# Kernel tuning notes

Measured on AMD Instinct MI355X. Metric: run time of the kernel, lower is better.

The kernel has to match this reference:

```python
import jax, jax.numpy as jnp
import numpy as np

N = 50000
E = 1600000
IN_C = 128
HID_C = 128
OUT_C = 64
NUM_REL = 8
NUM_BASES = 4


def rgcn_conv(x, edge_index, edge_type, basis, comp, root, bias):
    """Faithful PyG RGCNConv with basis decomposition and mean aggregation.

    basis: (num_bases, in, out); comp: (num_rel, num_bases);
    root: (in, out); bias: (out,).
    """
    # Compose per-relation weights from bases: W_r = sum_b comp[r,b] * basis[b]
    W = jnp.einsum('rb,bio->rio', comp, basis)  # (R, in, out)
    src, dst = edge_index[0], edge_index[1]
    # Segment id encodes (relation, dst node) so one segment_sum handles all relations
    seg = edge_type * N + dst  # (E,)
    msgs = x[src]  # (E, in) gather
    sums = jax.ops.segment_sum(msgs, seg, num_segments=NUM_REL * N)
    cnt = jax.ops.segment_sum(jnp.ones((seg.shape[0],), dtype=x.dtype), seg,
                              num_segments=NUM_REL * N)
    mean = sums / jnp.maximum(cnt, 1.0)[:, None]  # mean aggr; empty segs -> 0
    agg = mean.reshape(NUM_REL, N, -1)  # (R, N, in)
    out = jnp.einsum('rni,rio->no', agg, W)
    out = out + x @ root + bias  # root/self-loop weight + bias
    return out


def setup_inputs() -> dict:
    key = jax.random.key(0)
    ks = jax.random.split(key, 12)
    x = jax.random.normal(ks[0], (N, IN_C), dtype=jnp.float32)
    A = jax.random.randint(ks[1], (2, E), 0, N, dtype=jnp.int64)
    edge_type = jax.random.randint(ks[2], (E,), 0, NUM_REL, dtype=jnp.int64)
    def glorot(k, shape):
        fan_in, fan_out = shape[-2], shape[-1]
        lim = jnp.sqrt(6.0 / (fan_in + fan_out)).astype(jnp.float32)
        return jax.random.uniform(k, shape, jnp.float32, -lim, lim)
    w1_basis = glorot(ks[3], (NUM_BASES, IN_C, HID_C))
    w1_comp = glorot(ks[4], (NUM_REL, NUM_BASES))
    w1_root = glorot(ks[5], (IN_C, HID_C))
    w1_bias = jnp.zeros((HID_C,), jnp.float32)
    w2_basis = glorot(ks[6], (NUM_BASES, HID_C, OUT_C))
    w2_comp = glorot(ks[7], (NUM_REL, NUM_BASES))
    w2_root = glorot(ks[8], (HID_C, OUT_C))
    w2_bias = jnp.zeros((OUT_C,), jnp.float32)
    return {"x": x, "A": A, "edge_type": edge_type,
            "w1_basis": w1_basis, "w1_comp": w1_comp, "w1_root": w1_root, "w1_bias": w1_bias,
            "w2_basis": w2_basis, "w2_comp": w2_comp, "w2_root": w2_root, "w2_bias": w2_bias}


def reference(x, A, edge_type, w1_basis, w1_comp, w1_root, w1_bias,
              w2_basis, w2_comp, w2_root, w2_bias):
    h = rgcn_conv(x, A, edge_type, w1_basis, w1_comp, w1_root, w1_bias)
    h = jax.nn.relu(h)
    out = rgcn_conv(h, A, edge_type, w2_basis, w2_comp, w2_root, w2_bias)
    return out
```

## Files before the change

### kernel.cpp

```cpp
#include <hip/hip_runtime.h>


#define N_NODES 50000
#define N_EDGES 1600000
#define N_REL   8
#define CAP     32
#define NSEG    (N_REL * N_NODES)

typedef __attribute__((ext_vector_type(8))) short short8;
typedef __attribute__((ext_vector_type(4))) float f32x4;

__device__ __forceinline__ ushort f2bf(float x) {
    unsigned u = __builtin_bit_cast(unsigned, x);
    u += 0x7FFFu + ((u >> 16) & 1u);
    return (ushort)(u >> 16);
}
__device__ __forceinline__ float u2f(unsigned u) {
    return __builtin_bit_cast(float, u);
}

__global__ void zero_i32_kernel(int* __restrict__ p, int n) {
    int i = blockIdx.x * 256 + threadIdx.x;
    if (i < n) p[i] = 0;
}

__global__ void to_bf16_kernel(const float* __restrict__ in,
                               ushort* __restrict__ out) {
    int i = blockIdx.x * 256 + threadIdx.x;
    int total = (N_NODES + 1) * 16;
    if (i >= total) return;
    int base = i * 8;
    short8 v;
    if (base < N_NODES * 128) {
        f32x4 a = *(const f32x4*)(in + base);
        f32x4 b = *(const f32x4*)(in + base + 4);
        v = (short8){(short)f2bf(a.x), (short)f2bf(a.y), (short)f2bf(a.z),
                     (short)f2bf(a.w), (short)f2bf(b.x), (short)f2bf(b.y),
                     (short)f2bf(b.z), (short)f2bf(b.w)};
    } else {
        v = (short8){0, 0, 0, 0, 0, 0, 0, 0};
    }
    *(short8*)(out + base) = v;
}

__global__ void compose_wt_kernel(const float* __restrict__ basis,
                                  const float* __restrict__ comp,
                                  const float* __restrict__ root,
                                  ushort* __restrict__ Wt,
                                  int outc, int total) {
    int i = blockIdx.x * 256 + threadIdx.x;
    if (i >= total) return;
    int per_r = outc << 7;
    int r = i / per_r;
    int rem = i - r * per_r;
    int n = rem >> 7;
    int k = rem & 127;
    float s;
    if (r == N_REL) {
        s = root[k * outc + n];
    } else {
        s = 0.f;
#pragma unroll
        for (int b = 0; b < 4; ++b)
            s += comp[r * 4 + b] * basis[(b * 128 + k) * outc + n];
    }
    Wt[i] = f2bf(s);
}

__global__ void build_ell_kernel(const int* __restrict__ A,
                                 const int* __restrict__ etype,
                                 int* __restrict__ cnt,
                                 ushort* __restrict__ ell) {
    int e = blockIdx.x * 256 + threadIdx.x;
    if (e >= N_EDGES) return;
    int s = __builtin_nontemporal_load(A + e);
    int d = __builtin_nontemporal_load(A + N_EDGES + e);
    int t = __builtin_nontemporal_load(etype + e);
    int seg = t * N_NODES + d;
    int slot = atomicAdd(&cnt[seg], 1);
    if (slot < CAP) ell[(size_t)seg * CAP + slot] = (ushort)s;
}

template <int OUTC, bool RELU, bool BF16OUT>
__global__ __launch_bounds__(256, 8)
void rgcn_layer_mfma(const ushort* __restrict__ xbf,
                     const int* __restrict__ cnt,
                     const ushort* __restrict__ ell,
                     const ushort* __restrict__ Wt,
                     const float* __restrict__ bias,
                     void* __restrict__ outp) {
    constexpr int LDK = 136;
    constexpr int TN  = 32;
    constexpr int NCH = OUTC / 32;

    __shared__ ushort meanT[TN * LDK];
    __shared__ ushort Wl[32 * LDK];

    const int tid   = threadIdx.x;
    const int lane  = tid & 63;
    const int wave  = tid >> 6;
    const int nbase = blockIdx.x * TN;

    const int g  = tid >> 4;
    const int j  = tid & 15;
    const int j8 = j * 8;
    const int gb = lane & 48;

    const int rt = wave & 1;
    const int ch = wave >> 1;
    const int lr = lane & 15;
    const int kc = (lane >> 4) * 8;

    f32x4 acc[NCH];
#pragma unroll
    for (int t = 0; t < NCH; ++t) acc[t] = (f32x4){0.f, 0.f, 0.f, 0.f};

    for (int r = 0; r <= N_REL; ++r) {
#pragma unroll
        for (int p = 0; p < 2; ++p) {
            int a  = p * 16 + g;
            int gn = nbase + a;
            short8 sv = (short8){0, 0, 0, 0, 0, 0, 0, 0};
            if (gn < N_NODES) {
                if (r == N_REL) {
                    sv = *(const short8*)(xbf + (size_t)gn * 128 + j8);
                } else {
                    int seg = r * N_NODES + gn;
                    int c   = cnt[seg];
                    int cc  = c < CAP ? c : CAP;
                    uint pre = *(const uint*)(ell + (size_t)seg * CAP + 2 * j);
                    f32x4 s0 = (f32x4){0.f, 0.f, 0.f, 0.f};
                    f32x4 s1 = (f32x4){0.f, 0.f, 0.f, 0.f};
                    int ccr = (cc + 3) & ~3;
                    for (int e = 0; e < ccr; e += 4) {
                        uint ua = __shfl(pre, gb + (e >> 1), 64);
                        uint ub = __shfl(pre, gb + (e >> 1) + 1, 64);
                        int i0 = (e + 0 < cc) ? (int)(ua & 0xFFFFu) : N_NODES;
                        int i1 = (e + 1 < cc) ? (int)(ua >> 16)     : N_NODES;
                        int i2 = (e + 2 < cc) ? (int)(ub & 0xFFFFu) : N_NODES;
                        int i3 = (e + 3 < cc) ? (int)(ub >> 16)     : N_NODES;
                        short8 v0 = *(const short8*)(xbf + (size_t)i0 * 128 + j8);
                        short8 v1 = *(const short8*)(xbf + (size_t)i1 * 128 + j8);
                        short8 v2 = *(const short8*)(xbf + (size_t)i2 * 128 + j8);
                        short8 v3 = *(const short8*)(xbf + (size_t)i3 * 128 + j8);
#pragma unroll
                        for (int u = 0; u < 4; ++u) {
                            short8 v = (u == 0) ? v0 : (u == 1) ? v1
                                     : (u == 2) ? v2 : v3;
                            uint4 w = __builtin_bit_cast(uint4, v);
                            s0.x += u2f(w.x << 16);
                            s0.y += u2f(w.x & 0xFFFF0000u);
                            s0.z += u2f(w.y << 16);
                            s0.w += u2f(w.y & 0xFFFF0000u);
                            s1.x += u2f(w.z << 16);
                            s1.y += u2f(w.z & 0xFFFF0000u);
                            s1.z += u2f(w.w << 16);
                            s1.w += u2f(w.w & 0xFFFF0000u);
                        }
                    }
                    float inv = 1.f / (float)(c > 1 ? c : 1);
                    s0 *= inv;
                    s1 *= inv;
                    sv = (short8){(short)f2bf(s0.x), (short)f2bf(s0.y),
                                  (short)f2bf(s0.z), (short)f2bf(s0.w),
                                  (short)f2bf(s1.x), (short)f2bf(s1.y),
                                  (short)f2bf(s1.z), (short)f2bf(s1.w)};
                }
            }
            *(short8*)&meanT[a * LDK + j8] = sv;
        }
        __syncthreads();

        short8 af[4];
        const int m = rt * 16 + lr;
#pragma unroll
        for (int ks = 0; ks < 4; ++ks)
            af[ks] = *(const short8*)&meanT[m * LDK + ks * 32 + kc];

#pragma unroll
        for (int c = 0; c < NCH; ++c) {
            {
                const float4* src =
                    (const float4*)(Wt + ((size_t)r * OUTC + c * 32) * 128);
#pragma unroll
                for (int q = 0; q < 2; ++q) {
                    int idx = tid + q * 256;
                    int n   = idx >> 4;
                    int k8  = idx & 15;
                    *(float4*)&Wl[n * LDK + k8 * 8] = src[idx];
                }
            }
            __syncthreads();
            const int n = ch * 16 + lr;
            f32x4 a = acc[c];
#pragma unroll
            for (int ks = 0; ks < 4; ++ks) {
                short8 bf = *(const short8*)&Wl[n * LDK + ks * 32 + kc];
                a = __builtin_amdgcn_mfma_f32_16x16x32_bf16(af[ks], bf, a,
                                                            0, 0, 0);
            }
            acc[c] = a;
            if (c + 1 < NCH) __syncthreads();
        }
    }

    const int rq = (lane >> 4) * 4;
#pragma unroll
    for (int t = 0; t < NCH; ++t) {
        int col  = t * 32 + ch * 16 + lr;
        float bv = bias[col];
#pragma unroll
        for (int q = 0; q < 4; ++q) {
            int node = nbase + rt * 16 + rq + q;
            if (node < N_NODES) {
                float v = acc[t][q] + bv;
                if (RELU) v = fmaxf(v, 0.f);
                if (BF16OUT)
                    __builtin_nontemporal_store(
                        f2bf(v), (ushort*)outp + (size_t)node * OUTC + col);
                else
                    __builtin_nontemporal_store(
                        v, (float*)outp + (size_t)node * OUTC + col);
            }
        }
    }
}

extern "C" void kernel_launch(void* const* d_in, const int* in_sizes, int n_in,
                              void* d_out, int out_size, void* d_ws, size_t ws_size,
                              hipStream_t stream) {
    const float* x        = (const float*)d_in[0];
    const int*   A        = (const int*)d_in[1];
    const int*   etype    = (const int*)d_in[2];
    const float* w1_basis = (const float*)d_in[3];
    const float* w1_comp  = (const float*)d_in[4];
    const float* w1_root  = (const float*)d_in[5];
    const float* w1_bias  = (const float*)d_in[6];
    const float* w2_basis = (const float*)d_in[7];
    const float* w2_comp  = (const float*)d_in[8];
    const float* w2_root  = (const float*)d_in[9];
    const float* w2_bias  = (const float*)d_in[10];
    float* out = (float*)d_out;

    char* ws = (char*)d_ws;
    ushort* Wt1  = (ushort*)(ws);
    ushort* Wt2  = (ushort*)(ws + (512 << 10));
    int*    cnt  = (int*)(ws + (1 << 20));
    ushort* x_bf = (ushort*)(ws + (3ull << 20));
    ushort* h_bf = (ushort*)(ws + (16ull << 20));
    ushort* ell  = (ushort*)(ws + (29ull << 20));

    zero_i32_kernel<<<(NSEG + 255) / 256, 256, 0, stream>>>(cnt, NSEG);
    to_bf16_kernel<<<((N_NODES + 1) * 16 + 255) / 256, 256, 0, stream>>>(x, x_bf);
    zero_i32_kernel<<<1, 64, 0, stream>>>((int*)(h_bf + (size_t)N_NODES * 128), 64);
    compose_wt_kernel<<<(9 * 128 * 128 + 255) / 256, 256, 0, stream>>>(
        w1_basis, w1_comp, w1_root, Wt1, 128, 9 * 128 * 128);
    compose_wt_kernel<<<(9 * 64 * 128 + 255) / 256, 256, 0, stream>>>(
        w2_basis, w2_comp, w2_root, Wt2, 64, 9 * 64 * 128);
    build_ell_kernel<<<(N_EDGES + 255) / 256, 256, 0, stream>>>(A, etype, cnt, ell);

    int grid = (N_NODES + 31) / 32;
    rgcn_layer_mfma<128, true, true><<<grid, 256, 0, stream>>>(
        x_bf, cnt, ell, Wt1, w1_bias, h_bf);
    rgcn_layer_mfma<64, false, false><<<grid, 256, 0, stream>>>(
        h_bf, cnt, ell, Wt2, w2_bias, out);
}
```

Baseline: 369.9 us.

## Double node tile to 64 with 512-thread blocks and fuse setup kernels

```diff
diff --git a/kernel.cpp b/kernel.cpp
--- a/kernel.cpp
+++ b/kernel.cpp
@@ -25,34 +25,57 @@
 }
 
 __global__ void to_bf16_kernel(const float* __restrict__ in,
-                               ushort* __restrict__ out) {
+                               ushort* __restrict__ out,
+                               ushort* __restrict__ hbf) {
     int i = blockIdx.x * 256 + threadIdx.x;
-    int total = (N_NODES + 1) * 16;
-    if (i >= total) return;
-    int base = i * 8;
-    short8 v;
-    if (base < N_NODES * 128) {
-        f32x4 a = *(const f32x4*)(in + base);
-        f32x4 b = *(const f32x4*)(in + base + 4);
-        v = (short8){(short)f2bf(a.x), (short)f2bf(a.y), (short)f2bf(a.z),
-                     (short)f2bf(a.w), (short)f2bf(b.x), (short)f2bf(b.y),
-                     (short)f2bf(b.z), (short)f2bf(b.w)};
+    int totx = (N_NODES + 1) * 16;
+    if (i < totx) {
+        int base = i * 8;
+        short8 v;
+        if (base < N_NODES * 128) {
+            f32x4 a = *(const f32x4*)(in + base);
+            f32x4 b = *(const f32x4*)(in + base + 4);
+            v = (short8){(short)f2bf(a.x), (short)f2bf(a.y), (short)f2bf(a.z),
+                         (short)f2bf(a.w), (short)f2bf(b.x), (short)f2bf(b.y),
+                         (short)f2bf(b.z), (short)f2bf(b.w)};
+        } else {
+            v = (short8){0, 0, 0, 0, 0, 0, 0, 0};
+        }
+        *(short8*)(out + base) = v;
+    } else if (i < totx + 16) {
+        int idx = i - totx;
+        *(short8*)(hbf + (size_t)N_NODES * 128 + idx * 8) =
+            (short8){0, 0, 0, 0, 0, 0, 0, 0};
+    }
+}
+
+__global__ void compose_wt_kernel(const float* __restrict__ basis1,
+                                  const float* __restrict__ comp1,
+                                  const float* __restrict__ root1,
+                                  const float* __restrict__ basis2,
+                                  const float* __restrict__ comp2,
+                                  const float* __restrict__ root2,
+                                  ushort* __restrict__ Wt1,
+                                  ushort* __restrict__ Wt2) {
+    constexpr int T1 = 9 * 128 * 128;
+    constexpr int T2 = 9 * 64 * 128;
+    int i = blockIdx.x * 256 + threadIdx.x;
+    if (i >= T1 + T2) return;
+    const float* basis;
+    const float* comp;
+    const float* root;
+    ushort* Wt;
+    int outc, ii;
+    if (i < T1) {
+        basis = basis1; comp = comp1; root = root1; Wt = Wt1;
+        outc = 128; ii = i;
     } else {
-        v = (short8){0, 0, 0, 0, 0, 0, 0, 0};
-    }
-    *(short8*)(out + base) = v;
-}
-
-__global__ void compose_wt_kernel(const float* __restrict__ basis,
-                                  const float* __restrict__ comp,
-                                  const float* __restrict__ root,
-                                  ushort* __restrict__ Wt,
-                                  int outc, int total) {
-    int i = blockIdx.x * 256 + threadIdx.x;
-    if (i >= total) return;
+        basis = basis2; comp = comp2; root = root2; Wt = Wt2;
+        outc = 64; ii = i - T1;
+    }
     int per_r = outc << 7;
-    int r = i / per_r;
-    int rem = i - r * per_r;
+    int r = ii / per_r;
+    int rem = ii - r * per_r;
     int n = rem >> 7;
     int k = rem & 127;
     float s;
@@ -64,7 +87,7 @@
         for (int b = 0; b < 4; ++b)
             s += comp[r * 4 + b] * basis[(b * 128 + k) * outc + n];
     }
-    Wt[i] = f2bf(s);
+    Wt[ii] = f2bf(s);
 }
 
 __global__ void build_ell_kernel(const int* __restrict__ A,
@@ -82,7 +105,7 @@
 }
 
 template <int OUTC, bool RELU, bool BF16OUT>
-__global__ __launch_bounds__(256, 8)
+__global__ __launch_bounds__(512, 8)
 void rgcn_layer_mfma(const ushort* __restrict__ xbf,
                      const int* __restrict__ cnt,
                      const ushort* __restrict__ ell,
@@ -90,7 +113,7 @@
                      const float* __restrict__ bias,
                      void* __restrict__ outp) {
     constexpr int LDK = 136;
-    constexpr int TN  = 32;
+    constexpr int TN  = 64;
     constexpr int NCH = OUTC / 32;
 
     __shared__ ushort meanT[TN * LDK];
@@ -106,8 +129,8 @@
     const int j8 = j * 8;
     const int gb = lane & 48;
 
-    const int rt = wave & 1;
-    const int ch = wave >> 1;
+    const int rt = wave & 3;
+    const int ch = wave >> 2;
     const int lr = lane & 15;
     const int kc = (lane >> 4) * 8;
 
@@ -118,7 +141,7 @@
     for (int r = 0; r <= N_REL; ++r) {
 #pragma unroll
         for (int p = 0; p < 2; ++p) {
-            int a  = p * 16 + g;
+            int a  = p * 32 + g;
             int gn = nbase + a;
             short8 sv = (short8){0, 0, 0, 0, 0, 0, 0, 0};
             if (gn < N_NODES) {
@@ -182,13 +205,9 @@
             {
                 const float4* src =
                     (const float4*)(Wt + ((size_t)r * OUTC + c * 32) * 128);
-#pragma unroll
-                for (int q = 0; q < 2; ++q) {
-                    int idx = tid + q * 256;
-                    int n   = idx >> 4;
-                    int k8  = idx & 15;
-                    *(float4*)&Wl[n * LDK + k8 * 8] = src[idx];
-                }
+                int n  = tid >> 4;
+                int k8 = tid & 15;
+                *(float4*)&Wl[n * LDK + k8 * 8] = src[tid];
             }
             __syncthreads();
             const int n = ch * 16 + lr;
@@ -251,17 +270,16 @@
     ushort* ell  = (ushort*)(ws + (29ull << 20));
 
     zero_i32_kernel<<<(NSEG + 255) / 256, 256, 0, stream>>>(cnt, NSEG);
-    to_bf16_kernel<<<((N_NODES + 1) * 16 + 255) / 256, 256, 0, stream>>>(x, x_bf);
-    zero_i32_kernel<<<1, 64, 0, stream>>>((int*)(h_bf + (size_t)N_NODES * 128), 64);
-    compose_wt_kernel<<<(9 * 128 * 128 + 255) / 256, 256, 0, stream>>>(
-        w1_basis, w1_comp, w1_root, Wt1, 128, 9 * 128 * 128);
-    compose_wt_kernel<<<(9 * 64 * 128 + 255) / 256, 256, 0, stream>>>(
-        w2_basis, w2_comp, w2_root, Wt2, 64, 9 * 64 * 128);
+    to_bf16_kernel<<<((N_NODES + 1) * 16 + 16 + 255) / 256, 256, 0, stream>>>(
+        x, x_bf, h_bf);
+    compose_wt_kernel<<<(9 * 128 * 128 + 9 * 64 * 128 + 255) / 256, 256, 0,
+                      stream>>>(w1_basis, w1_comp, w1_root,
+                                w2_basis, w2_comp, w2_root, Wt1, Wt2);
     build_ell_kernel<<<(N_EDGES + 255) / 256, 256, 0, stream>>>(A, etype, cnt, ell);
 
-    int grid = (N_NODES + 31) / 32;
-    rgcn_layer_mfma<128, true, true><<<grid, 256, 0, stream>>>(
+    int grid = (N_NODES + 63) / 64;
+    rgcn_layer_mfma<128, true, true><<<grid, 512, 0, stream>>>(
         x_bf, cnt, ell, Wt1, w1_bias, h_bf);
-    rgcn_layer_mfma<64, false, false><<<grid, 256, 0, stream>>>(
+    rgcn_layer_mfma<64, false, false><<<grid, 512, 0, stream>>>(
         h_bf, cnt, ell, Wt2, w2_bias, out);
 }
```

Measured after the change: 368.8 us. Within noise of the previous version (-0.3%).
